# Performance work log

Measured on AMD Instinct MI355X. Metric: run time of the kernel, lower is better.

Reference implementation:

```python
import jax, jax.numpy as jnp
import numpy as np

N_NODES = 100000
N_PART = 5000
N_EDGES = 1000000
D_NODE = 128
D_PART = 128
D_ATT = 20


def setup_inputs() -> dict:
    key = jax.random.key(0)
    ks = jax.random.split(key, 20)
    inp = {
        "nodes_hidden": jax.random.normal(ks[0], (N_NODES, D_NODE), jnp.float32),
        "particles_hidden": jax.random.normal(ks[1], (N_PART, D_PART), jnp.float32),
        "global_rep": jax.random.normal(ks[2], (N_PART, D_NODE), jnp.float32),
        "src": jax.random.randint(ks[3], (N_EDGES,), 0, N_NODES, jnp.int32),
        "dst": jax.random.randint(ks[4], (N_EDGES,), 0, N_PART, jnp.int32),
        "key_W": jax.random.normal(ks[5], (D_NODE, D_ATT), jnp.float32) * 0.05,
        "key_b": jnp.zeros((D_ATT,), jnp.float32),
        "val_W": jax.random.normal(ks[6], (D_NODE, D_PART), jnp.float32) * 0.05,
        "val_b": jnp.zeros((D_PART,), jnp.float32),
        "q_W": jax.random.normal(ks[7], (D_PART + D_NODE, D_ATT), jnp.float32) * 0.05,
        "q_b": jnp.zeros((D_ATT,), jnp.float32),
        "W_ih": jax.random.normal(ks[8], (3 * D_PART, D_PART), jnp.float32) * 0.05,
        "W_hh": jax.random.normal(ks[9], (3 * D_PART, D_PART), jnp.float32) * 0.05,
        "b_ih": jnp.zeros((3 * D_PART,), jnp.float32),
        "b_hh": jnp.zeros((3 * D_PART,), jnp.float32),
        "ln_g": jnp.ones((D_PART,), jnp.float32),
        "ln_b": jnp.zeros((D_PART,), jnp.float32),
        "mlp_W1": jax.random.normal(ks[10], (D_PART, 64), jnp.float32) * 0.05,
        "mlp_b1": jnp.zeros((64,), jnp.float32),
        "mlp_W2": jax.random.normal(ks[11], (64, D_PART), jnp.float32) * 0.05,
        "mlp_b2": jnp.zeros((D_PART,), jnp.float32),
    }
    return inp


def reference(nodes_hidden, particles_hidden, global_rep, src, dst,
              key_W, key_b, val_W, val_b, q_W, q_b,
              W_ih, W_hh, b_ih, b_hh, ln_g, ln_b,
              mlp_W1, mlp_b1, mlp_W2, mlp_b2):
    norm = jnp.float32(1.0) / jnp.sqrt(jnp.float32(D_ATT))
    keys = nodes_hidden @ key_W + key_b          # [N, 20]
    vals = nodes_hidden @ val_W + val_b          # [N, P]
    q_in = jnp.concatenate([particles_hidden, global_rep], axis=1)
    query = q_in @ q_W + q_b                     # [Np, 20]

    # per-edge raw attention (ReLU'd copy in edges.data is unused downstream)
    att = jnp.sum(keys[src] * query[dst], axis=1) * norm     # [E]
    msg = att[:, None] * vals[src]                            # [E, P]
    weighted_sum = jax.ops.segment_sum(msg, dst, num_segments=particles_hidden.shape[0])

    # GRUCell(input=weighted_sum, hidden=particles_hidden), torch semantics
    gi = weighted_sum @ W_ih.T + b_ih
    gh = particles_hidden @ W_hh.T + b_hh
    i_r, i_z, i_n = jnp.split(gi, 3, axis=1)
    h_r, h_z, h_n = jnp.split(gh, 3, axis=1)
    r = jax.nn.sigmoid(i_r + h_r)
    z = jax.nn.sigmoid(i_z + h_z)
    n = jnp.tanh(i_n + r * h_n)
    h_new = (1.0 - z) * n + z * particles_hidden

    # LayerNorm (eps=1e-5)
    mu = jnp.mean(h_new, axis=-1, keepdims=True)
    var = jnp.mean(jnp.square(h_new - mu), axis=-1, keepdims=True)
    ln = (h_new - mu) * jax.lax.rsqrt(var + 1e-5) * ln_g + ln_b

    mlp_out = jax.nn.relu(ln @ mlp_W1 + mlp_b1) @ mlp_W2 + mlp_b2
    return particles_hidden + mlp_out
```

## Files before the change

kernel.cpp:

```cpp
#include <hip/hip_runtime.h>
#include <hip/hip_fp16.h>
#include <math.h>

#define N_NODES 100000
#define N_PART  5000
#define N_EDGES 1000000
#define D_NODE  128
#define D_PART  128
#define D_ATT   20
#define NBLK    128
#define EPB     ((N_EDGES + NBLK - 1) / NBLK)
#define TPV3    10

__device__ __forceinline__ float sigmoid_(float x) { return 1.f / (1.f + __expf(-x)); }
__device__ __forceinline__ float tanh_(float x)    { return 1.f - 2.f / (__expf(2.f * x) + 1.f); }

__global__ __launch_bounds__(256) void build_wbig_dot_kernel(
    const float* __restrict__ valW, const float* __restrict__ Wih,
    float* __restrict__ Wbig)
{
    __shared__ float s_a[32][128];
    __shared__ float s_b[64][128];
    int kt = blockIdx.x / 6, jt = blockIdx.x % 6;
    int k0 = kt * 32, j0 = jt * 64;
    int t = threadIdx.x;

    for (int f = t; f < 32 * 32; f += 256) {
        int r = f >> 5, c4 = (f & 31) * 4;
        *(float4*)&s_a[r][c4] = *(const float4*)(valW + (size_t)(k0 + r) * 128 + c4);
    }
    for (int f = t; f < 64 * 32; f += 256) {
        int r = f >> 5, c4 = (f & 31) * 4;
        *(float4*)&s_b[r][c4] = *(const float4*)(Wih + (size_t)(j0 + r) * 128 + c4);
    }
    __syncthreads();

    #pragma unroll
    for (int f = 0; f < 8; f++) {
        int idx = t + f * 256;
        int kk = idx >> 6, jj = idx & 63;
        float acc = 0.f;
        #pragma unroll 8
        for (int m = 0; m < 128; m++) acc += s_a[kk][m] * s_b[jj][m];
        Wbig[(size_t)(k0 + kk) * 512 + j0 + jj] = acc;
    }
    if (jt == 0) {
        for (int f = t; f < 32 * 128; f += 256) {
            int kk = f >> 7, jj = 384 + (f & 127);
            Wbig[(size_t)(k0 + kk) * 512 + jj] = 0.f;
        }
    }
}

__global__ __launch_bounds__(256) void build_wbig_copy_kernel(
    const float* __restrict__ Whh, float* __restrict__ Wbig)
{
    int idx = blockIdx.x * 256 + threadIdx.x;
    int kp = idx >> 9;
    int j = idx & 511;
    float v = 0.f;
    if (j < 256)       v = Whh[j * 128 + kp];
    else if (j >= 384) v = Whh[(j - 128) * 128 + kp];
    Wbig[(size_t)(128 + kp) * 512 + j] = v;
}

__global__ __launch_bounds__(256) void build_bvec_kernel(
    const float* __restrict__ valb, const float* __restrict__ Wih,
    float* __restrict__ bvec)
{
    int c = blockIdx.x * 256 + threadIdx.x;
    if (c < 384) {
        float acc = 0.f;
        #pragma unroll 8
        for (int m = 0; m < 128; m++) acc += valb[m] * Wih[c * 128 + m];
        bvec[c] = acc;
    }
}

__global__ __launch_bounds__(256) void nodes_to_half_kernel(
    const float* __restrict__ nodes, __half* __restrict__ nh)
{
    int i = blockIdx.x * 256 + threadIdx.x;
    if (i < N_NODES * D_NODE / 4) {
        float4 v = ((const float4*)nodes)[i];
        __half2 a = __floats2half2_rn(v.x, v.y);
        __half2 b = __floats2half2_rn(v.z, v.w);
        ((__half2*)nh)[i * 2]     = a;
        ((__half2*)nh)[i * 2 + 1] = b;
    }
}

__global__ __launch_bounds__(256) void query_qk_v2(
    const float* __restrict__ ph, const float* __restrict__ gr,
    const float* __restrict__ qW, const float* __restrict__ qb,
    const float* __restrict__ keyW, const float* __restrict__ keyb,
    float* __restrict__ qk, float* __restrict__ qoff)
{
    __shared__ float s_in[32][256];
    __shared__ float s_qW[256 * 20];
    __shared__ float s_kWT[20][128];
    __shared__ float s_q[32][20];

    int t = threadIdx.x;
    int pbase = blockIdx.x * 32;

    for (int f = t; f < 32 * 64; f += 256) {
        int pl = f >> 6, c4 = (f & 63) * 4;
        int p = min(pbase + pl, N_PART - 1);
        float4 v;
        if (c4 < 128) v = *(const float4*)(ph + (size_t)p * 128 + c4);
        else          v = *(const float4*)(gr + (size_t)p * 128 + (c4 - 128));
        *(float4*)&s_in[pl][c4] = v;
    }
    for (int f = t; f < 1280; f += 256)
        *(float4*)&s_qW[f * 4] = *(const float4*)(qW + f * 4);
    for (int f = t; f < 2560; f += 256) {
        int j = f / 20, a = f % 20;
        s_kWT[a][j] = keyW[f];
    }
    __syncthreads();

    for (int idx = t; idx < 32 * 20; idx += 256) {
        int pl = idx / 20, a = idx % 20;
        float acc = qb[a];
        #pragma unroll 8
        for (int k = 0; k < 256; k++) acc += s_in[pl][k] * s_qW[k * 20 + a];
        s_q[pl][a] = acc;
    }
    __syncthreads();

    for (int idx = t; idx < 32 * 128; idx += 256) {
        int pl = idx >> 7, j = idx & 127;
        int p = pbase + pl;
        if (p < N_PART) {
            float acc = 0.f;
            #pragma unroll
            for (int a = 0; a < D_ATT; a++) acc += s_kWT[a][j] * s_q[pl][a];
            qk[(size_t)p * 128 + j] = acc;
        }
    }
    if (t < 32) {
        int p = pbase + t;
        if (p < N_PART) {
            float o = 0.f;
            #pragma unroll
            for (int a = 0; a < D_ATT; a++) o += keyb[a] * s_q[t][a];
            qoff[p] = o;
        }
    }
}

__global__ __launch_bounds__(256) void block_hist_kernel(
    const int* __restrict__ dst, int* __restrict__ blockhist)
{
    __shared__ int h[N_PART];
    int b = blockIdx.x;
    for (int i = threadIdx.x; i < N_PART; i += 256) h[i] = 0;
    __syncthreads();
    int beg = b * EPB, end = min(beg + EPB, N_EDGES);
    for (int e = beg + threadIdx.x; e < end; e += 256)
        atomicAdd(&h[dst[e]], 1);
    __syncthreads();
    for (int i = threadIdx.x; i < N_PART; i += 256)
        blockhist[(size_t)b * N_PART + i] = h[i];
}

__global__ __launch_bounds__(256) void colscan_kernel(
    int* __restrict__ blockhist, int* __restrict__ totals)
{
    int i = blockIdx.x * 256 + threadIdx.x;
    if (i >= N_PART) return;
    int run = 0;
    for (int b = 0; b < NBLK; b++) {
        size_t idx = (size_t)b * N_PART + i;
        int v = blockhist[idx];
        blockhist[idx] = run;
        run += v;
    }
    totals[i] = run;
}

__global__ __launch_bounds__(256) void scan_kernel(
    const int* __restrict__ totals, int* __restrict__ offsets)
{
    __shared__ int ss[256];
    int t = threadIdx.x;
    const int CH = 20;
    int beg = t * CH;
    int end = min(beg + CH, N_PART);
    int lsum = 0;
    for (int i = beg; i < end; i++) lsum += totals[i];
    ss[t] = lsum;
    __syncthreads();
    for (int off = 1; off < 256; off <<= 1) {
        int v = (t >= off) ? ss[t - off] : 0;
        __syncthreads();
        ss[t] += v;
        __syncthreads();
    }
    int base = ss[t] - lsum;
    for (int i = beg; i < end; i++) {
        offsets[i] = base;
        base += totals[i];
    }
    if (t == 0) offsets[N_PART] = N_EDGES;
}

__global__ __launch_bounds__(256) void scatter_sorted_kernel(
    const int* __restrict__ src, const int* __restrict__ dst,
    const int* __restrict__ offsets, const int* __restrict__ blockhist,
    int* __restrict__ ssrc)
{
    __shared__ int cur[N_PART];
    int b = blockIdx.x;
    for (int i = threadIdx.x; i < N_PART; i += 256)
        cur[i] = offsets[i] + blockhist[(size_t)b * N_PART + i];
    __syncthreads();
    int beg = b * EPB, end = min(beg + EPB, N_EDGES);
    for (int e = beg + threadIdx.x; e < end; e += 256) {
        int d = dst[e];
        int pos = atomicAdd(&cur[d], 1);
        ssrc[pos] = src[e];
    }
}

__global__ __launch_bounds__(256) void edge_agg_f16(
    const __half* __restrict__ nh, const float* __restrict__ qk,
    const float* __restrict__ qoff,
    const int* __restrict__ offsets, const int* __restrict__ ssrc,
    float* __restrict__ agg, float* __restrict__ att_sum)
{
    const float norm = 0.22360679774997896f;
    int p = blockIdx.x;
    int tid = threadIdx.x;
    int lane = tid & 63;
    int wave = tid >> 6;
    int lane16 = lane & 15;
    int col8 = lane16 * 8;

    float4 q0 = *(const float4*)(qk + (size_t)p * 128 + col8);
    float4 q1 = *(const float4*)(qk + (size_t)p * 128 + col8 + 4);
    float qo = qoff[p];
    int beg = offsets[p];
    int n = offsets[p + 1] - beg;

    float4 a0 = {0.f, 0.f, 0.f, 0.f};
    float4 a1 = {0.f, 0.f, 0.f, 0.f};
    float asum = 0.f;

    int i = wave * 8 + (lane >> 4);
    for (; i + 4 < n; i += 32) {
        int sA = ssrc[beg + i];
        int sB = ssrc[beg + i + 4];
        float4 rawA = *(const float4*)(nh + (size_t)sA * 128 + col8);
        float4 rawB = *(const float4*)(nh + (size_t)sB * 128 + col8);
        const __half2* hA = (const __half2*)&rawA;
        const __half2* hB = (const __half2*)&rawB;
        float2 xa0 = __half22float2(hA[0]), xa1 = __half22float2(hA[1]);
        float2 xa2 = __half22float2(hA[2]), xa3 = __half22float2(hA[3]);
        float2 xb0 = __half22float2(hB[0]), xb1 = __half22float2(hB[1]);
        float2 xb2 = __half22float2(hB[2]), xb3 = __half22float2(hB[3]);
        float dA = xa0.x * q0.x + xa0.y * q0.y + xa1.x * q0.z + xa1.y * q0.w
                 + xa2.x * q1.x + xa2.y * q1.y + xa3.x * q1.z + xa3.y * q1.w;
        float dB = xb0.x * q0.x + xb0.y * q0.y + xb1.x * q0.z + xb1.y * q0.w
                 + xb2.x * q1.x + xb2.y * q1.y + xb3.x * q1.z + xb3.y * q1.w;
        #pragma unroll
        for (int off = 1; off <= 8; off <<= 1) {
            dA += __shfl_xor(dA, off, 64);
            dB += __shfl_xor(dB, off, 64);
        }
        float attA = (dA + qo) * norm;
        float attB = (dB + qo) * norm;
        a0.x += attA * xa0.x + attB * xb0.x;
        a0.y += attA * xa0.y + attB * xb0.y;
        a0.z += attA * xa1.x + attB * xb1.x;
        a0.w += attA * xa1.y + attB * xb1.y;
        a1.x += attA * xa2.x + attB * xb2.x;
        a1.y += attA * xa2.y + attB * xb2.y;
        a1.z += attA * xa3.x + attB * xb3.x;
        a1.w += attA * xa3.y + attB * xb3.y;
        asum += attA + attB;
    }
    if (i < n) {
        int sA = ssrc[beg + i];
        float4 rawA = *(const float4*)(nh + (size_t)sA * 128 + col8);
        const __half2* hA = (const __half2*)&rawA;
        float2 xa0 = __half22float2(hA[0]), xa1 = __half22float2(hA[1]);
        float2 xa2 = __half22float2(hA[2]), xa3 = __half22float2(hA[3]);
        float dA = xa0.x * q0.x + xa0.y * q0.y + xa1.x * q0.z + xa1.y * q0.w
                 + xa2.x * q1.x + xa2.y * q1.y + xa3.x * q1.z + xa3.y * q1.w;
        #pragma unroll
        for (int off = 1; off <= 8; off <<= 1) dA += __shfl_xor(dA, off, 64);
        float attA = (dA + qo) * norm;
        a0.x += attA * xa0.x; a0.y += attA * xa0.y;
        a0.z += attA * xa1.x; a0.w += attA * xa1.y;
        a1.x += attA * xa2.x; a1.y += attA * xa2.y;
        a1.z += attA * xa3.x; a1.w += attA * xa3.y;
        asum += attA;
    }

    #pragma unroll
    for (int off = 16; off <= 32; off <<= 1) {
        a0.x += __shfl_xor(a0.x, off, 64);
        a0.y += __shfl_xor(a0.y, off, 64);
        a0.z += __shfl_xor(a0.z, off, 64);
        a0.w += __shfl_xor(a0.w, off, 64);
        a1.x += __shfl_xor(a1.x, off, 64);
        a1.y += __shfl_xor(a1.y, off, 64);
        a1.z += __shfl_xor(a1.z, off, 64);
        a1.w += __shfl_xor(a1.w, off, 64);
        asum += __shfl_xor(asum, off, 64);
    }

    __shared__ float s_part[4][128];
    __shared__ float s_as[4];
    if (lane < 16) {
        *(float4*)&s_part[wave][col8]     = a0;
        *(float4*)&s_part[wave][col8 + 4] = a1;
        if (lane == 0) s_as[wave] = asum;
    }
    __syncthreads();

    if (tid < 128) {
        float v = s_part[0][tid] + s_part[1][tid] + s_part[2][tid] + s_part[3][tid];
        agg[(size_t)p * 128 + tid] = v;
        if (tid == 0) att_sum[p] = s_as[0] + s_as[1] + s_as[2] + s_as[3];
    }
}

__global__ __launch_bounds__(256) void edge_agg_f32(
    const float* __restrict__ nodes, const float* __restrict__ qk,
    const float* __restrict__ qoff,
    const int* __restrict__ offsets, const int* __restrict__ ssrc,
    float* __restrict__ agg, float* __restrict__ att_sum)
{
    const float norm = 0.22360679774997896f;
    int p = blockIdx.x;
    int tid = threadIdx.x;
    int lane = tid & 63;
    int wave = tid >> 6;
    int half = lane >> 5;
    int colq = (lane & 31) * 4;

    const float4 q = *(const float4*)(qk + (size_t)p * 128 + colq);
    float qo = qoff[p];
    int beg = offsets[p], end = offsets[p + 1];
    int n = end - beg;
    int np = (n + 1) >> 1;
    int npfull = n >> 1;

    float4 a = {0.f, 0.f, 0.f, 0.f};
    float asum = 0.f;

    int pi = wave;
    for (; pi + 12 < npfull; pi += 16) {
        int e0 = beg + 2 * pi + half;
        int s0 = ssrc[e0];
        int s1 = ssrc[e0 + 8];
        int s2 = ssrc[e0 + 16];
        int s3 = ssrc[e0 + 24];
        float4 x0 = *(const float4*)(nodes + (size_t)s0 * 128 + colq);
        float4 x1 = *(const float4*)(nodes + (size_t)s1 * 128 + colq);
        float4 x2 = *(const float4*)(nodes + (size_t)s2 * 128 + colq);
        float4 x3 = *(const float4*)(nodes + (size_t)s3 * 128 + colq);
        float d0 = x0.x * q.x + x0.y * q.y + x0.z * q.z + x0.w * q.w;
        float d1 = x1.x * q.x + x1.y * q.y + x1.z * q.z + x1.w * q.w;
        float d2 = x2.x * q.x + x2.y * q.y + x2.z * q.z + x2.w * q.w;
        float d3 = x3.x * q.x + x3.y * q.y + x3.z * q.z + x3.w * q.w;
        #pragma unroll
        for (int off = 1; off <= 16; off <<= 1) {
            d0 += __shfl_xor(d0, off, 64);
            d1 += __shfl_xor(d1, off, 64);
            d2 += __shfl_xor(d2, off, 64);
            d3 += __shfl_xor(d3, off, 64);
        }
        float t0 = (d0 + qo) * norm;
        float t1 = (d1 + qo) * norm;
        float t2 = (d2 + qo) * norm;
        float t3 = (d3 + qo) * norm;
        a.x += t0 * x0.x + t1 * x1.x + t2 * x2.x + t3 * x3.x;
        a.y += t0 * x0.y + t1 * x1.y + t2 * x2.y + t3 * x3.y;
        a.z += t0 * x0.z + t1 * x1.z + t2 * x2.z + t3 * x3.z;
        a.w += t0 * x0.w + t1 * x1.w + t2 * x2.w + t3 * x3.w;
        asum += t0 + t1 + t2 + t3;
    }
    for (; pi < np; pi += 4) {
        int e0 = beg + 2 * pi;
        bool has1 = (e0 + 1 < end);
        int s0 = ssrc[e0];
        int s1 = has1 ? ssrc[e0 + 1] : s0;
        int s = half ? s1 : s0;
        float4 x = *(const float4*)(nodes + (size_t)s * 128 + colq);
        float d = x.x * q.x + x.y * q.y + x.z * q.z + x.w * q.w;
        #pragma unroll
        for (int off = 1; off <= 16; off <<= 1) d += __shfl_xor(d, off, 64);
        float att = (d + qo) * norm;
        if (half && !has1) att = 0.f;
        a.x += att * x.x; a.y += att * x.y; a.z += att * x.z; a.w += att * x.w;
        asum += att;
    }

    a.x += __shfl_xor(a.x, 32, 64);
    a.y += __shfl_xor(a.y, 32, 64);
    a.z += __shfl_xor(a.z, 32, 64);
    a.w += __shfl_xor(a.w, 32, 64);
    asum += __shfl_xor(asum, 32, 64);

    __shared__ float s_acc[4][128];
    __shared__ float s_as[4];
    if (lane < 32) {
        *(float4*)&s_acc[wave][colq] = a;
        if (lane == 0) s_as[wave] = asum;
    }
    __syncthreads();

    if (tid < 128) {
        float v = s_acc[0][tid] + s_acc[1][tid] + s_acc[2][tid] + s_acc[3][tid];
        agg[(size_t)p * 128 + tid] = v;
        if (tid == 0) att_sum[p] = s_as[0] + s_as[1] + s_as[2] + s_as[3];
    }
}

__global__ __launch_bounds__(256) void gru_fused_v4(
    const float* __restrict__ agg, const float* __restrict__ att_sum,
    const float* __restrict__ ph,
    const float* __restrict__ Wbig, const float* __restrict__ bvec,
    const float* __restrict__ bih, const float* __restrict__ bhh,
    const float* __restrict__ lng, const float* __restrict__ lnb,
    const float* __restrict__ W1, const float* __restrict__ b1,
    const float* __restrict__ W2, const float* __restrict__ b2,
    float* __restrict__ out)
{
    __shared__ float s_in[TPV3][256];
    __shared__ float s_acc[TPV3][512];
    __shared__ float s_ln[TPV3][128];
    __shared__ float s_hid[TPV3][64];

    int t = threadIdx.x;
    int pbase = blockIdx.x * TPV3;

    for (int f = t; f < TPV3 * 64; f += 256) {
        int pl = f >> 6, c4 = (f & 63) * 4;
        int p = pbase + pl;
        float4 v;
        if (c4 < 128) v = *(const float4*)(agg + (size_t)p * 128 + c4);
        else          v = *(const float4*)(ph + (size_t)p * 128 + (c4 - 128));
        *(float4*)&s_in[pl][c4] = v;
    }

    int jq = t & 127;
    int j4 = jq * 4;
    int pg = t >> 7;
    float4 cb, bv;
    if (j4 < 256) {
        float4 bi = *(const float4*)(bih + j4);
        float4 bh = *(const float4*)(bhh + j4);
        cb.x = bi.x + bh.x; cb.y = bi.y + bh.y; cb.z = bi.z + bh.z; cb.w = bi.w + bh.w;
        bv = *(const float4*)(bvec + j4);
    } else if (j4 < 384) {
        cb = *(const float4*)(bih + j4);
        bv = *(const float4*)(bvec + j4);
    } else {
        cb = *(const float4*)(bhh + (j4 - 128));
        bv.x = bv.y = bv.z = bv.w = 0.f;
    }
    float4 acc[5];
    #pragma unroll
    for (int i = 0; i < 5; i++) {
        float as = att_sum[pbase + pg * 5 + i];
        acc[i].x = cb.x + as * bv.x;
        acc[i].y = cb.y + as * bv.y;
        acc[i].z = cb.z + as * bv.z;
        acc[i].w = cb.w + as * bv.w;
    }
    __syncthreads();

    #pragma unroll 4
    for (int k = 0; k < 256; k++) {
        float4 w = *(const float4*)(Wbig + (size_t)k * 512 + j4);
        #pragma unroll
        for (int i = 0; i < 5; i++) {
            float x = s_in[pg * 5 + i][k];
            acc[i].x += x * w.x; acc[i].y += x * w.y;
            acc[i].z += x * w.z; acc[i].w += x * w.w;
        }
    }

    #pragma unroll
    for (int i = 0; i < 5; i++)
        *(float4*)&s_acc[pg * 5 + i][j4] = acc[i];
    __syncthreads();

    for (int idx = t; idx < TPV3 * 32; idx += 256) {
        int pl = idx >> 5, q = idx & 31;
        int c4 = q * 4;
        float4 r4 = *(const float4*)&s_acc[pl][c4];
        float4 z4 = *(const float4*)&s_acc[pl][128 + c4];
        float4 i4 = *(const float4*)&s_acc[pl][256 + c4];
        float4 n4 = *(const float4*)&s_acc[pl][384 + c4];
        float4 h4 = *(const float4*)&s_in[pl][128 + c4];
        float r0 = sigmoid_(r4.x), r1 = sigmoid_(r4.y), r2 = sigmoid_(r4.z), r3 = sigmoid_(r4.w);
        float z0 = sigmoid_(z4.x), z1 = sigmoid_(z4.y), z2 = sigmoid_(z4.z), z3 = sigmoid_(z4.w);
        float n0 = tanh_(i4.x + r0 * n4.x), n1 = tanh_(i4.y + r1 * n4.y);
        float n2 = tanh_(i4.z + r2 * n4.z), n3 = tanh_(i4.w + r3 * n4.w);
        float4 hn;
        hn.x = (1.f - z0) * n0 + z0 * h4.x;
        hn.y = (1.f - z1) * n1 + z1 * h4.y;
        hn.z = (1.f - z2) * n2 + z2 * h4.z;
        hn.w = (1.f - z3) * n3 + z3 * h4.w;
        *(float4*)&s_ln[pl][c4] = hn;
    }
    __syncthreads();

    {
        int wv = t >> 6, l = t & 63;
        for (int pl = wv; pl < TPV3; pl += 4) {
            float v0 = s_ln[pl][l * 2], v1 = s_ln[pl][l * 2 + 1];
            float sum = v0 + v1, sq = v0 * v0 + v1 * v1;
            #pragma unroll
            for (int off = 1; off <= 32; off <<= 1) {
                sum += __shfl_xor(sum, off, 64);
                sq  += __shfl_xor(sq, off, 64);
            }
            float mu = sum * (1.f / 128.f);
            float var = sq * (1.f / 128.f) - mu * mu;
            float rstd = rsqrtf(var + 1e-5f);
            s_ln[pl][l * 2]     = (v0 - mu) * rstd * lng[l * 2] + lnb[l * 2];
            s_ln[pl][l * 2 + 1] = (v1 - mu) * rstd * lng[l * 2 + 1] + lnb[l * 2 + 1];
        }
    }
    __syncthreads();

    for (int idx = t; idx < TPV3 * 64; idx += 256) {
        int pl = idx >> 6, u = idx & 63;
        float a0 = b1[u];
        #pragma unroll 4
        for (int k = 0; k < 128; k++) a0 += s_ln[pl][k] * W1[k * 64 + u];
        s_hid[pl][u] = fmaxf(a0, 0.f);
    }
    __syncthreads();

    for (int idx = t; idx < TPV3 * 32; idx += 256) {
        int pl = idx >> 5, q = idx & 31;
        int c4 = q * 4;
        float4 o = *(const float4*)(b2 + c4);
        #pragma unroll 4
        for (int u = 0; u < 64; u++) {
            float av = s_hid[pl][u];
            float4 w = *(const float4*)(W2 + u * 128 + c4);
            o.x += av * w.x; o.y += av * w.y; o.z += av * w.z; o.w += av * w.w;
        }
        float4 h4 = *(const float4*)&s_in[pl][128 + c4];
        float4 res;
        res.x = h4.x + o.x; res.y = h4.y + o.y;
        res.z = h4.z + o.z; res.w = h4.w + o.w;
        *(float4*)(out + (size_t)(pbase + pl) * 128 + c4) = res;
    }
}

extern "C" void kernel_launch(void* const* d_in, const int* in_sizes, int n_in,
                              void* d_out, int out_size, void* d_ws, size_t ws_size,
                              hipStream_t stream) {
    const float* nodes = (const float*)d_in[0];
    const float* ph    = (const float*)d_in[1];
    const float* gr    = (const float*)d_in[2];
    const int*   src   = (const int*)d_in[3];
    const int*   dst   = (const int*)d_in[4];
    const float* keyW  = (const float*)d_in[5];
    const float* keyb  = (const float*)d_in[6];
    const float* valW  = (const float*)d_in[7];
    const float* valb  = (const float*)d_in[8];
    const float* qW    = (const float*)d_in[9];
    const float* qb    = (const float*)d_in[10];
    const float* Wih   = (const float*)d_in[11];
    const float* Whh   = (const float*)d_in[12];
    const float* bih   = (const float*)d_in[13];
    const float* bhh   = (const float*)d_in[14];
    const float* lng   = (const float*)d_in[15];
    const float* lnb   = (const float*)d_in[16];
    const float* W1    = (const float*)d_in[17];
    const float* b1    = (const float*)d_in[18];
    const float* W2    = (const float*)d_in[19];
    const float* b2    = (const float*)d_in[20];
    float* out = (float*)d_out;

    float* ws_f      = (float*)d_ws;
    float* qk        = ws_f;
    float* qoff      = qk + 640000;
    float* agg       = qoff + 5008;
    float* att_sum   = agg + 640000;
    float* Wbig      = att_sum + 5008;
    float* bvec      = Wbig + 131072;
    int*   totals    = (int*)(bvec + 512);
    int*   offsets   = totals + 5008;
    int*   blockhist = offsets + 5008;
    int*   ssrc      = blockhist + (size_t)NBLK * N_PART;
    __half* nodes_h  = (__half*)(ssrc + 1000000);

    size_t base_floats = 640000 + 5008 + 640000 + 5008 + 131072 + 512
                       + 5008 + 5008 + (size_t)NBLK * N_PART + 1000000;
    size_t need_f16 = base_floats * sizeof(float) + (size_t)N_NODES * D_NODE * sizeof(__half);
    bool use_f16 = (ws_size >= need_f16);

    build_wbig_dot_kernel<<<24, 256, 0, stream>>>(valW, Wih, Wbig);
    build_wbig_copy_kernel<<<256, 256, 0, stream>>>(Whh, Wbig);
    build_bvec_kernel<<<2, 256, 0, stream>>>(valb, Wih, bvec);
    query_qk_v2<<<(N_PART + 31) / 32, 256, 0, stream>>>(ph, gr, qW, qb, keyW, keyb, qk, qoff);
    block_hist_kernel<<<NBLK, 256, 0, stream>>>(dst, blockhist);
    colscan_kernel<<<(N_PART + 255) / 256, 256, 0, stream>>>(blockhist, totals);
    scan_kernel<<<1, 256, 0, stream>>>(totals, offsets);
    scatter_sorted_kernel<<<NBLK, 256, 0, stream>>>(src, dst, offsets, blockhist, ssrc);
    if (use_f16) {
        nodes_to_half_kernel<<<(N_NODES * D_NODE / 4 + 255) / 256, 256, 0, stream>>>(nodes, nodes_h);
        edge_agg_f16<<<N_PART, 256, 0, stream>>>(nodes_h, qk, qoff, offsets, ssrc, agg, att_sum);
    } else {
        edge_agg_f32<<<N_PART, 256, 0, stream>>>(nodes, qk, qoff, offsets, ssrc, agg, att_sum);
    }
    gru_fused_v4<<<N_PART / TPV3, 256, 0, stream>>>(
        agg, att_sum, ph, Wbig, bvec, bih, bhh, lng, lnb, W1, b1, W2, b2, out);
}
```

Baseline: 326.5 us.

## Merge setup kernels, fuse sort passes with grid barriers, split GRU stage

```diff
diff --git a/kernel.cpp b/kernel.cpp
--- a/kernel.cpp
+++ b/kernel.cpp
@@ -8,219 +8,222 @@
 #define D_NODE  128
 #define D_PART  128
 #define D_ATT   20
-#define NBLK    128
-#define EPB     ((N_EDGES + NBLK - 1) / NBLK)
-#define TPV3    10
+#define SORTB   128
+#define EPB     ((N_EDGES + SORTB - 1) / SORTB)
+
+#define CONV_END  12500
+#define DOT_END   (CONV_END + 192)
+#define COPY_END  (DOT_END + 256)
+#define ZF_END    (COPY_END + 64)
+#define BINIT_END (ZF_END + 2)
+#define MB_END    (BINIT_END + 128)
+#define MK_END    (MB_END + 1)
+#define SETUP_GRID MK_END
 
 __device__ __forceinline__ float sigmoid_(float x) { return 1.f / (1.f + __expf(-x)); }
 __device__ __forceinline__ float tanh_(float x)    { return 1.f - 2.f / (__expf(2.f * x) + 1.f); }
 
-__global__ __launch_bounds__(256) void build_wbig_dot_kernel(
+__global__ __launch_bounds__(256) void mega_setup(
+    const float* __restrict__ nodes, __half* __restrict__ nh, int use_f16,
     const float* __restrict__ valW, const float* __restrict__ Wih,
-    float* __restrict__ Wbig)
+    const float* __restrict__ Whh, const float* __restrict__ valb,
+    const float* __restrict__ bih, const float* __restrict__ bhh,
+    const float* __restrict__ qW, const float* __restrict__ qb,
+    const float* __restrict__ keyW, const float* __restrict__ keyb,
+    float* __restrict__ Wbig2, float* __restrict__ binit,
+    float* __restrict__ bvec4, float* __restrict__ M,
+    float* __restrict__ mkbuf)
 {
-    __shared__ float s_a[32][128];
-    __shared__ float s_b[64][128];
-    int kt = blockIdx.x / 6, jt = blockIdx.x % 6;
-    int k0 = kt * 32, j0 = jt * 64;
+    int b = blockIdx.x;
     int t = threadIdx.x;
 
-    for (int f = t; f < 32 * 32; f += 256) {
-        int r = f >> 5, c4 = (f & 31) * 4;
-        *(float4*)&s_a[r][c4] = *(const float4*)(valW + (size_t)(k0 + r) * 128 + c4);
-    }
-    for (int f = t; f < 64 * 32; f += 256) {
-        int r = f >> 5, c4 = (f & 31) * 4;
-        *(float4*)&s_b[r][c4] = *(const float4*)(Wih + (size_t)(j0 + r) * 128 + c4);
-    }
-    __syncthreads();
-
-    #pragma unroll
-    for (int f = 0; f < 8; f++) {
-        int idx = t + f * 256;
-        int kk = idx >> 6, jj = idx & 63;
+    if (b < CONV_END) {
+        if (!use_f16) return;
+        int i = b * 256 + t;
+        float4 v = ((const float4*)nodes)[i];
+        __half2 a = __floats2half2_rn(v.x, v.y);
+        __half2 c = __floats2half2_rn(v.z, v.w);
+        ((__half2*)nh)[i * 2]     = a;
+        ((__half2*)nh)[i * 2 + 1] = c;
+    } else if (b < DOT_END) {
+        int idx = (b - CONV_END) * 256 + t;
+        int k = idx / 384, c = idx % 384;
+        const float* va = valW + (size_t)k * 128;
+        const float* wb = Wih + (size_t)c * 128;
         float acc = 0.f;
         #pragma unroll 8
-        for (int m = 0; m < 128; m++) acc += s_a[kk][m] * s_b[jj][m];
-        Wbig[(size_t)(k0 + kk) * 512 + j0 + jj] = acc;
-    }
-    if (jt == 0) {
-        for (int f = t; f < 32 * 128; f += 256) {
-            int kk = f >> 7, jj = 384 + (f & 127);
-            Wbig[(size_t)(k0 + kk) * 512 + jj] = 0.f;
-        }
-    }
-}
-
-__global__ __launch_bounds__(256) void build_wbig_copy_kernel(
-    const float* __restrict__ Whh, float* __restrict__ Wbig)
-{
-    int idx = blockIdx.x * 256 + threadIdx.x;
-    int kp = idx >> 9;
-    int j = idx & 511;
-    float v = 0.f;
-    if (j < 256)       v = Whh[j * 128 + kp];
-    else if (j >= 384) v = Whh[(j - 128) * 128 + kp];
-    Wbig[(size_t)(128 + kp) * 512 + j] = v;
-}
-
-__global__ __launch_bounds__(256) void build_bvec_kernel(
-    const float* __restrict__ valb, const float* __restrict__ Wih,
-    float* __restrict__ bvec)
-{
-    int c = blockIdx.x * 256 + threadIdx.x;
-    if (c < 384) {
+        for (int m = 0; m < 128; m++) acc += va[m] * wb[m];
+        Wbig2[(size_t)k * 512 + (c & 127) * 4 + (c >> 7)] = acc;
+    } else if (b < COPY_END) {
+        int idx = (b - DOT_END) * 256 + t;
+        int kp = idx >> 9, rem = idx & 511;
+        int j = rem >> 2, g = rem & 3;
+        float v = 0.f;
+        if (g < 2)       v = Whh[(size_t)(g * 128 + j) * 128 + kp];
+        else if (g == 3) v = Whh[(size_t)(256 + j) * 128 + kp];
+        Wbig2[(size_t)(128 + kp) * 512 + rem] = v;
+    } else if (b < ZF_END) {
+        int idx = (b - COPY_END) * 256 + t;
+        int k = idx >> 7, j = idx & 127;
+        Wbig2[(size_t)k * 512 + j * 4 + 3] = 0.f;
+    } else if (b < BINIT_END) {
+        int idx = (b - ZF_END) * 256 + t;
+        int j = idx >> 2, g = idx & 3;
+        float bi;
+        if (g == 0)      bi = bih[j] + bhh[j];
+        else if (g == 1) bi = bih[128 + j] + bhh[128 + j];
+        else if (g == 2) bi = bih[256 + j];
+        else             bi = bhh[256 + j];
+        binit[idx] = bi;
+        float bv = 0.f;
+        if (g < 3) {
+            const float* wr = Wih + (size_t)(g * 128 + j) * 128;
+            #pragma unroll 8
+            for (int m = 0; m < 128; m++) bv += valb[m] * wr[m];
+        }
+        bvec4[idx] = bv;
+    } else if (b < MB_END) {
+        int idx = (b - BINIT_END) * 256 + t;
+        int k = idx >> 7, j = idx & 127;
+        const float* qr = qW + k * 20;
+        const float* kr = keyW + j * 20;
         float acc = 0.f;
-        #pragma unroll 8
-        for (int m = 0; m < 128; m++) acc += valb[m] * Wih[c * 128 + m];
-        bvec[c] = acc;
-    }
-}
-
-__global__ __launch_bounds__(256) void nodes_to_half_kernel(
-    const float* __restrict__ nodes, __half* __restrict__ nh)
-{
-    int i = blockIdx.x * 256 + threadIdx.x;
-    if (i < N_NODES * D_NODE / 4) {
-        float4 v = ((const float4*)nodes)[i];
-        __half2 a = __floats2half2_rn(v.x, v.y);
-        __half2 b = __floats2half2_rn(v.z, v.w);
-        ((__half2*)nh)[i * 2]     = a;
-        ((__half2*)nh)[i * 2 + 1] = b;
-    }
-}
-
-__global__ __launch_bounds__(256) void query_qk_v2(
-    const float* __restrict__ ph, const float* __restrict__ gr,
-    const float* __restrict__ qW, const float* __restrict__ qb,
-    const float* __restrict__ keyW, const float* __restrict__ keyb,
-    float* __restrict__ qk, float* __restrict__ qoff)
-{
-    __shared__ float s_in[32][256];
-    __shared__ float s_qW[256 * 20];
-    __shared__ float s_kWT[20][128];
-    __shared__ float s_q[32][20];
-
-    int t = threadIdx.x;
-    int pbase = blockIdx.x * 32;
-
-    for (int f = t; f < 32 * 64; f += 256) {
-        int pl = f >> 6, c4 = (f & 63) * 4;
-        int p = min(pbase + pl, N_PART - 1);
-        float4 v;
-        if (c4 < 128) v = *(const float4*)(ph + (size_t)p * 128 + c4);
-        else          v = *(const float4*)(gr + (size_t)p * 128 + (c4 - 128));
-        *(float4*)&s_in[pl][c4] = v;
-    }
-    for (int f = t; f < 1280; f += 256)
-        *(float4*)&s_qW[f * 4] = *(const float4*)(qW + f * 4);
-    for (int f = t; f < 2560; f += 256) {
-        int j = f / 20, a = f % 20;
-        s_kWT[a][j] = keyW[f];
-    }
-    __syncthreads();
-
-    for (int idx = t; idx < 32 * 20; idx += 256) {
-        int pl = idx / 20, a = idx % 20;
-        float acc = qb[a];
-        #pragma unroll 8
-        for (int k = 0; k < 256; k++) acc += s_in[pl][k] * s_qW[k * 20 + a];
-        s_q[pl][a] = acc;
-    }
-    __syncthreads();
-
-    for (int idx = t; idx < 32 * 128; idx += 256) {
-        int pl = idx >> 7, j = idx & 127;
-        int p = pbase + pl;
-        if (p < N_PART) {
+        #pragma unroll
+        for (int a = 0; a < D_ATT; a++) acc += qr[a] * kr[a];
+        M[idx] = acc;
+    } else {
+        {
+            float acc = 0.f;
+            const float* qr = qW + t * 20;
+            #pragma unroll
+            for (int a = 0; a < D_ATT; a++) acc += qr[a] * keyb[a];
+            mkbuf[t] = acc;
+        }
+        if (t < 128) {
+            float acc = 0.f;
+            const float* kr = keyW + t * 20;
+            #pragma unroll
+            for (int a = 0; a < D_ATT; a++) acc += qb[a] * kr[a];
+            mkbuf[260 + t] = acc;
+        }
+        if (t == 0) {
             float acc = 0.f;
             #pragma unroll
-            for (int a = 0; a < D_ATT; a++) acc += s_kWT[a][j] * s_q[pl][a];
-            qk[(size_t)p * 128 + j] = acc;
-        }
-    }
-    if (t < 32) {
-        int p = pbase + t;
-        if (p < N_PART) {
-            float o = 0.f;
-            #pragma unroll
-            for (int a = 0; a < D_ATT; a++) o += keyb[a] * s_q[t][a];
+            for (int a = 0; a < D_ATT; a++) acc += qb[a] * keyb[a];
+            mkbuf[256] = acc;
+        }
+    }
+}
+
+__device__ __forceinline__ void gridbar(int* bar, int nblk) {
+    __syncthreads();
+    if (threadIdx.x == 0) {
+        __threadfence();
+        atomicAdd(bar, 1);
+        while (__hip_atomic_load(bar, __ATOMIC_ACQUIRE, __HIP_MEMORY_SCOPE_AGENT) < nblk) {}
+        __threadfence();
+    }
+    __syncthreads();
+}
+
+__global__ __launch_bounds__(256) void phase2_kernel(
+    const int* __restrict__ src, const int* __restrict__ dst,
+    const float* __restrict__ ph, const float* __restrict__ gr,
+    const float* __restrict__ M, const float* __restrict__ mkbuf,
+    int* __restrict__ blockhist, int* __restrict__ totals,
+    int* __restrict__ offsets, int* __restrict__ ssrc,
+    float* __restrict__ qk, float* __restrict__ qoff,
+    int* __restrict__ bar)
+{
+    __shared__ char smem[20000];
+    int t = threadIdx.x;
+
+    if (blockIdx.x < SORTB) {
+        int b = blockIdx.x;
+        int* h = (int*)smem;
+        for (int i = t; i < N_PART; i += 256) h[i] = 0;
+        __syncthreads();
+        int beg = b * EPB, end = min(beg + EPB, N_EDGES);
+        for (int e = beg + t; e < end; e += 256)
+            atomicAdd(&h[dst[e]], 1);
+        __syncthreads();
+        for (int i = t; i < N_PART; i += 256)
+            blockhist[(size_t)b * N_PART + i] = h[i];
+        gridbar(&bar[0], SORTB);
+
+        int gid = b * 256 + t;
+        if (gid < N_PART) {
+            int run = 0;
+            for (int bb = 0; bb < SORTB; bb++) {
+                size_t idx = (size_t)bb * N_PART + gid;
+                int v = blockhist[idx];
+                blockhist[idx] = run;
+                run += v;
+            }
+            totals[gid] = run;
+        }
+        gridbar(&bar[1], SORTB);
+
+        if (b == 0) {
+            __shared__ int ss[256];
+            const int CH = 20;
+            int sbeg = t * CH;
+            int send = min(sbeg + CH, N_PART);
+            int lsum = 0;
+            for (int i = sbeg; i < send; i++) lsum += totals[i];
+            ss[t] = lsum;
+            __syncthreads();
+            for (int off = 1; off < 256; off <<= 1) {
+                int v = (t >= off) ? ss[t - off] : 0;
+                __syncthreads();
+                ss[t] += v;
+                __syncthreads();
+            }
+            int base = ss[t] - lsum;
+            for (int i = sbeg; i < send; i++) {
+                offsets[i] = base;
+                base += totals[i];
+            }
+            if (t == 0) offsets[N_PART] = N_EDGES;
+        }
+        gridbar(&bar[2], SORTB);
+
+        for (int i = t; i < N_PART; i += 256)
+            h[i] = offsets[i] + blockhist[(size_t)b * N_PART + i];
+        __syncthreads();
+        for (int e = beg + t; e < end; e += 256) {
+            int d = dst[e];
+            int pos = atomicAdd(&h[d], 1);
+            ssrc[pos] = src[e];
+        }
+    } else {
+        float (*s_in)[256] = (float(*)[256])smem;
+        int pbase = (blockIdx.x - SORTB) * 8;
+        for (int f = t; f < 8 * 64; f += 256) {
+            int pl = f >> 6, c4 = (f & 63) * 4;
+            int p = pbase + pl;
+            float4 v;
+            if (c4 < 128) v = *(const float4*)(ph + (size_t)p * 128 + c4);
+            else          v = *(const float4*)(gr + (size_t)p * 128 + (c4 - 128));
+            *(float4*)&s_in[pl][c4] = v;
+        }
+        __syncthreads();
+        int pl = t >> 5, jq = t & 31;
+        int j4 = jq * 4;
+        int p = pbase + pl;
+        float4 acc = *(const float4*)(mkbuf + 260 + j4);
+        #pragma unroll 4
+        for (int k = 0; k < 256; k++) {
+            float x = s_in[pl][k];
+            float4 w = *(const float4*)(M + (size_t)k * 128 + j4);
+            acc.x += x * w.x; acc.y += x * w.y; acc.z += x * w.z; acc.w += x * w.w;
+        }
+        *(float4*)(qk + (size_t)p * 128 + j4) = acc;
+        if (jq == 0) {
+            float o = mkbuf[256];
+            for (int k = 0; k < 256; k++) o += s_in[pl][k] * mkbuf[k];
             qoff[p] = o;
         }
-    }
-}
-
-__global__ __launch_bounds__(256) void block_hist_kernel(
-    const int* __restrict__ dst, int* __restrict__ blockhist)
-{
-    __shared__ int h[N_PART];
-    int b = blockIdx.x;
-    for (int i = threadIdx.x; i < N_PART; i += 256) h[i] = 0;
-    __syncthreads();
-    int beg = b * EPB, end = min(beg + EPB, N_EDGES);
-    for (int e = beg + threadIdx.x; e < end; e += 256)
-        atomicAdd(&h[dst[e]], 1);
-    __syncthreads();
-    for (int i = threadIdx.x; i < N_PART; i += 256)
-        blockhist[(size_t)b * N_PART + i] = h[i];
-}
-
-__global__ __launch_bounds__(256) void colscan_kernel(
-    int* __restrict__ blockhist, int* __restrict__ totals)
-{
-    int i = blockIdx.x * 256 + threadIdx.x;
-    if (i >= N_PART) return;
-    int run = 0;
-    for (int b = 0; b < NBLK; b++) {
-        size_t idx = (size_t)b * N_PART + i;
-        int v = blockhist[idx];
-        blockhist[idx] = run;
-        run += v;
-    }
-    totals[i] = run;
-}
-
-__global__ __launch_bounds__(256) void scan_kernel(
-    const int* __restrict__ totals, int* __restrict__ offsets)
-{
-    __shared__ int ss[256];
-    int t = threadIdx.x;
-    const int CH = 20;
-    int beg = t * CH;
-    int end = min(beg + CH, N_PART);
-    int lsum = 0;
-    for (int i = beg; i < end; i++) lsum += totals[i];
-    ss[t] = lsum;
-    __syncthreads();
-    for (int off = 1; off < 256; off <<= 1) {
-        int v = (t >= off) ? ss[t - off] : 0;
-        __syncthreads();
-        ss[t] += v;
-        __syncthreads();
-    }
-    int base = ss[t] - lsum;
-    for (int i = beg; i < end; i++) {
-        offsets[i] = base;
-        base += totals[i];
-    }
-    if (t == 0) offsets[N_PART] = N_EDGES;
-}
-
-__global__ __launch_bounds__(256) void scatter_sorted_kernel(
-    const int* __restrict__ src, const int* __restrict__ dst,
-    const int* __restrict__ offsets, const int* __restrict__ blockhist,
-    int* __restrict__ ssrc)
-{
-    __shared__ int cur[N_PART];
-    int b = blockIdx.x;
-    for (int i = threadIdx.x; i < N_PART; i += 256)
-        cur[i] = offsets[i] + blockhist[(size_t)b * N_PART + i];
-    __syncthreads();
-    int beg = b * EPB, end = min(beg + EPB, N_EDGES);
-    for (int e = beg + threadIdx.x; e < end; e += 256) {
-        int d = dst[e];
-        int pos = atomicAdd(&cur[d], 1);
-        ssrc[pos] = src[e];
     }
 }
 
@@ -421,25 +424,18 @@
     }
 }
 
-__global__ __launch_bounds__(256) void gru_fused_v4(
+__global__ __launch_bounds__(256) void gru_gemm(
     const float* __restrict__ agg, const float* __restrict__ att_sum,
     const float* __restrict__ ph,
-    const float* __restrict__ Wbig, const float* __restrict__ bvec,
-    const float* __restrict__ bih, const float* __restrict__ bhh,
-    const float* __restrict__ lng, const float* __restrict__ lnb,
-    const float* __restrict__ W1, const float* __restrict__ b1,
-    const float* __restrict__ W2, const float* __restrict__ b2,
-    float* __restrict__ out)
+    const float* __restrict__ Wbig2, const float* __restrict__ binit,
+    const float* __restrict__ bvec4, float* __restrict__ hnew)
 {
-    __shared__ float s_in[TPV3][256];
-    __shared__ float s_acc[TPV3][512];
-    __shared__ float s_ln[TPV3][128];
-    __shared__ float s_hid[TPV3][64];
-
+    __shared__ float s_in[8][256];
     int t = threadIdx.x;
-    int pbase = blockIdx.x * TPV3;
-
-    for (int f = t; f < TPV3 * 64; f += 256) {
+    int pg = blockIdx.x >> 2, cg = blockIdx.x & 3;
+    int pbase = pg * 8;
+
+    for (int f = t; f < 8 * 64; f += 256) {
         int pl = f >> 6, c4 = (f & 63) * 4;
         int p = pbase + pl;
         float4 v;
@@ -448,114 +444,93 @@
         *(float4*)&s_in[pl][c4] = v;
     }
 
-    int jq = t & 127;
-    int j4 = jq * 4;
-    int pg = t >> 7;
-    float4 cb, bv;
-    if (j4 < 256) {
-        float4 bi = *(const float4*)(bih + j4);
-        float4 bh = *(const float4*)(bhh + j4);
-        cb.x = bi.x + bh.x; cb.y = bi.y + bh.y; cb.z = bi.z + bh.z; cb.w = bi.w + bh.w;
-        bv = *(const float4*)(bvec + j4);
-    } else if (j4 < 384) {
-        cb = *(const float4*)(bih + j4);
-        bv = *(const float4*)(bvec + j4);
-    } else {
-        cb = *(const float4*)(bhh + (j4 - 128));
-        bv.x = bv.y = bv.z = bv.w = 0.f;
-    }
-    float4 acc[5];
-    #pragma unroll
-    for (int i = 0; i < 5; i++) {
-        float as = att_sum[pbase + pg * 5 + i];
-        acc[i].x = cb.x + as * bv.x;
-        acc[i].y = cb.y + as * bv.y;
-        acc[i].z = cb.z + as * bv.z;
-        acc[i].w = cb.w + as * bv.w;
-    }
+    int pl = t >> 5, jq = t & 31;
+    int j = cg * 32 + jq;
+    float4 bi = *(const float4*)(binit + j * 4);
+    float4 bv = *(const float4*)(bvec4 + j * 4);
+    float asum = att_sum[pbase + pl];
+    float4 acc;
+    acc.x = bi.x + asum * bv.x;
+    acc.y = bi.y + asum * bv.y;
+    acc.z = bi.z + asum * bv.z;
+    acc.w = bi.w + asum * bv.w;
     __syncthreads();
 
+    const float* wp = Wbig2 + j * 4;
     #pragma unroll 4
     for (int k = 0; k < 256; k++) {
-        float4 w = *(const float4*)(Wbig + (size_t)k * 512 + j4);
-        #pragma unroll
-        for (int i = 0; i < 5; i++) {
-            float x = s_in[pg * 5 + i][k];
-            acc[i].x += x * w.x; acc[i].y += x * w.y;
-            acc[i].z += x * w.z; acc[i].w += x * w.w;
-        }
-    }
-
+        float4 w = *(const float4*)(wp + k * 512);
+        float x = s_in[pl][k];
+        acc.x += x * w.x; acc.y += x * w.y;
+        acc.z += x * w.z; acc.w += x * w.w;
+    }
+
+    float r = sigmoid_(acc.x);
+    float z = sigmoid_(acc.y);
+    float n = tanh_(acc.z + r * acc.w);
+    float h = s_in[pl][128 + j];
+    hnew[(size_t)(pbase + pl) * 128 + j] = (1.f - z) * n + z * h;
+}
+
+__global__ __launch_bounds__(256) void epilogue_kernel(
+    const float* __restrict__ hnew, const float* __restrict__ ph,
+    const float* __restrict__ lng, const float* __restrict__ lnb,
+    const float* __restrict__ W1, const float* __restrict__ b1,
+    const float* __restrict__ W2, const float* __restrict__ b2,
+    float* __restrict__ out)
+{
+    __shared__ float s_ln[8][128];
+    __shared__ float s_hid[8][64];
+    int t = threadIdx.x;
+    int pbase = blockIdx.x * 8;
+    int pl = t >> 5, jq = t & 31;
+    int j4 = jq * 4;
+    int p = pbase + pl;
+
+    float4 hn = *(const float4*)(hnew + (size_t)p * 128 + j4);
+    float sum = hn.x + hn.y + hn.z + hn.w;
+    float sq  = hn.x * hn.x + hn.y * hn.y + hn.z * hn.z + hn.w * hn.w;
     #pragma unroll
-    for (int i = 0; i < 5; i++)
-        *(float4*)&s_acc[pg * 5 + i][j4] = acc[i];
+    for (int off = 1; off <= 16; off <<= 1) {
+        sum += __shfl_xor(sum, off, 64);
+        sq  += __shfl_xor(sq, off, 64);
+    }
+    float mu = sum * (1.f / 128.f);
+    float var = sq * (1.f / 128.f) - mu * mu;
+    float rstd = rsqrtf(var + 1e-5f);
+    {
+        float4 g4 = *(const float4*)(lng + j4);
+        float4 b4 = *(const float4*)(lnb + j4);
+        float4 ln4;
+        ln4.x = (hn.x - mu) * rstd * g4.x + b4.x;
+        ln4.y = (hn.y - mu) * rstd * g4.y + b4.y;
+        ln4.z = (hn.z - mu) * rstd * g4.z + b4.z;
+        ln4.w = (hn.w - mu) * rstd * g4.w + b4.w;
+        *(float4*)&s_ln[pl][j4] = ln4;
+    }
     __syncthreads();
 
-    for (int idx = t; idx < TPV3 * 32; idx += 256) {
-        int pl = idx >> 5, q = idx & 31;
-        int c4 = q * 4;
-        float4 r4 = *(const float4*)&s_acc[pl][c4];
-        float4 z4 = *(const float4*)&s_acc[pl][128 + c4];
-        float4 i4 = *(const float4*)&s_acc[pl][256 + c4];
-        float4 n4 = *(const float4*)&s_acc[pl][384 + c4];
-        float4 h4 = *(const float4*)&s_in[pl][128 + c4];
-        float r0 = sigmoid_(r4.x), r1 = sigmoid_(r4.y), r2 = sigmoid_(r4.z), r3 = sigmoid_(r4.w);
-        float z0 = sigmoid_(z4.x), z1 = sigmoid_(z4.y), z2 = sigmoid_(z4.z), z3 = sigmoid_(z4.w);
-        float n0 = tanh_(i4.x + r0 * n4.x), n1 = tanh_(i4.y + r1 * n4.y);
-        float n2 = tanh_(i4.z + r2 * n4.z), n3 = tanh_(i4.w + r3 * n4.w);
-        float4 hn;
-        hn.x = (1.f - z0) * n0 + z0 * h4.x;
-        hn.y = (1.f - z1) * n1 + z1 * h4.y;
-        hn.z = (1.f - z2) * n2 + z2 * h4.z;
-        hn.w = (1.f - z3) * n3 + z3 * h4.w;
-        *(float4*)&s_ln[pl][c4] = hn;
-    }
-    __syncthreads();
-
-    {
-        int wv = t >> 6, l = t & 63;
-        for (int pl = wv; pl < TPV3; pl += 4) {
-            float v0 = s_ln[pl][l * 2], v1 = s_ln[pl][l * 2 + 1];
-            float sum = v0 + v1, sq = v0 * v0 + v1 * v1;
-            #pragma unroll
-            for (int off = 1; off <= 32; off <<= 1) {
-                sum += __shfl_xor(sum, off, 64);
-                sq  += __shfl_xor(sq, off, 64);
-            }
-            float mu = sum * (1.f / 128.f);
-            float var = sq * (1.f / 128.f) - mu * mu;
-            float rstd = rsqrtf(var + 1e-5f);
-            s_ln[pl][l * 2]     = (v0 - mu) * rstd * lng[l * 2] + lnb[l * 2];
-            s_ln[pl][l * 2 + 1] = (v1 - mu) * rstd * lng[l * 2 + 1] + lnb[l * 2 + 1];
-        }
-    }
-    __syncthreads();
-
-    for (int idx = t; idx < TPV3 * 64; idx += 256) {
-        int pl = idx >> 6, u = idx & 63;
+    for (int idx = t; idx < 8 * 64; idx += 256) {
+        int pl2 = idx >> 6, u = idx & 63;
         float a0 = b1[u];
         #pragma unroll 4
-        for (int k = 0; k < 128; k++) a0 += s_ln[pl][k] * W1[k * 64 + u];
-        s_hid[pl][u] = fmaxf(a0, 0.f);
+        for (int k = 0; k < 128; k++) a0 += s_ln[pl2][k] * W1[k * 64 + u];
+        s_hid[pl2][u] = fmaxf(a0, 0.f);
     }
     __syncthreads();
 
-    for (int idx = t; idx < TPV3 * 32; idx += 256) {
-        int pl = idx >> 5, q = idx & 31;
-        int c4 = q * 4;
-        float4 o = *(const float4*)(b2 + c4);
-        #pragma unroll 4
-        for (int u = 0; u < 64; u++) {
-            float av = s_hid[pl][u];
-            float4 w = *(const float4*)(W2 + u * 128 + c4);
-            o.x += av * w.x; o.y += av * w.y; o.z += av * w.z; o.w += av * w.w;
-        }
-        float4 h4 = *(const float4*)&s_in[pl][128 + c4];
-        float4 res;
-        res.x = h4.x + o.x; res.y = h4.y + o.y;
-        res.z = h4.z + o.z; res.w = h4.w + o.w;
-        *(float4*)(out + (size_t)(pbase + pl) * 128 + c4) = res;
-    }
+    float4 o = *(const float4*)(b2 + j4);
+    #pragma unroll 4
+    for (int u = 0; u < 64; u++) {
+        float av = s_hid[pl][u];
+        float4 w = *(const float4*)(W2 + u * 128 + j4);
+        o.x += av * w.x; o.y += av * w.y; o.z += av * w.z; o.w += av * w.w;
+    }
+    float4 h4 = *(const float4*)(ph + (size_t)p * 128 + j4);
+    float4 res;
+    res.x = h4.x + o.x; res.y = h4.y + o.y;
+    res.z = h4.z + o.z; res.w = h4.w + o.w;
+    *(float4*)(out + (size_t)p * 128 + j4) = res;
 }
 
 extern "C" void kernel_launch(void* const* d_in, const int* in_sizes, int n_in,
@@ -584,38 +559,44 @@
     const float* b2    = (const float*)d_in[20];
     float* out = (float*)d_out;
 
-    float* ws_f      = (float*)d_ws;
-    float* qk        = ws_f;
-    float* qoff      = qk + 640000;
-    float* agg       = qoff + 5008;
-    float* att_sum   = agg + 640000;
-    float* Wbig      = att_sum + 5008;
-    float* bvec      = Wbig + 131072;
-    int*   totals    = (int*)(bvec + 512);
-    int*   offsets   = totals + 5008;
-    int*   blockhist = offsets + 5008;
-    int*   ssrc      = blockhist + (size_t)NBLK * N_PART;
-    __half* nodes_h  = (__half*)(ssrc + 1000000);
-
-    size_t base_floats = 640000 + 5008 + 640000 + 5008 + 131072 + 512
-                       + 5008 + 5008 + (size_t)NBLK * N_PART + 1000000;
-    size_t need_f16 = base_floats * sizeof(float) + (size_t)N_NODES * D_NODE * sizeof(__half);
-    bool use_f16 = (ws_size >= need_f16);
-
-    build_wbig_dot_kernel<<<24, 256, 0, stream>>>(valW, Wih, Wbig);
-    build_wbig_copy_kernel<<<256, 256, 0, stream>>>(Whh, Wbig);
-    build_bvec_kernel<<<2, 256, 0, stream>>>(valb, Wih, bvec);
-    query_qk_v2<<<(N_PART + 31) / 32, 256, 0, stream>>>(ph, gr, qW, qb, keyW, keyb, qk, qoff);
-    block_hist_kernel<<<NBLK, 256, 0, stream>>>(dst, blockhist);
-    colscan_kernel<<<(N_PART + 255) / 256, 256, 0, stream>>>(blockhist, totals);
-    scan_kernel<<<1, 256, 0, stream>>>(totals, offsets);
-    scatter_sorted_kernel<<<NBLK, 256, 0, stream>>>(src, dst, offsets, blockhist, ssrc);
+    float* ws_f    = (float*)d_ws;
+    float* qk      = ws_f;
+    float* qoff    = qk + 640000;
+    float* agg     = qoff + 5008;
+    float* att_sum = agg + 640000;
+    float* Wbig2   = att_sum + 5008;
+    float* binit   = Wbig2 + 131072;
+    float* bvec4   = binit + 512;
+    float* mkbuf   = bvec4 + 512;
+    float* M_      = mkbuf + 400;
+    int*   totals  = (int*)(M_ + 32768);
+    int*   offsets = totals + 5008;
+    int*   bar     = offsets + 5008;
+    int*   blockhist = bar + 16;
+    int*   ssrc    = blockhist + (size_t)SORTB * N_PART;
+    __half* nodes_h = (__half*)(ssrc + 1000000);
+
+    size_t base_floats = 640000 + 5008 + 640000 + 5008 + 131072 + 512 + 512 + 400
+                       + 32768 + 5008 + 5008 + 16 + (size_t)SORTB * N_PART + 1000000;
+    size_t need_f16 = base_floats * 4 + (size_t)N_NODES * D_NODE * sizeof(__half);
+    int use_f16 = (ws_size >= need_f16) ? 1 : 0;
+
+    hipMemsetAsync(bar, 0, 16 * sizeof(int), stream);
+
+    mega_setup<<<SETUP_GRID, 256, 0, stream>>>(
+        nodes, nodes_h, use_f16, valW, Wih, Whh, valb, bih, bhh,
+        qW, qb, keyW, keyb, Wbig2, binit, bvec4, M_, mkbuf);
+
+    phase2_kernel<<<SORTB + 625, 256, 0, stream>>>(
+        src, dst, ph, gr, M_, mkbuf, blockhist, totals, offsets, ssrc, qk, qoff, bar);
+
     if (use_f16) {
-        nodes_to_half_kernel<<<(N_NODES * D_NODE / 4 + 255) / 256, 256, 0, stream>>>(nodes, nodes_h);
         edge_agg_f16<<<N_PART, 256, 0, stream>>>(nodes_h, qk, qoff, offsets, ssrc, agg, att_sum);
     } else {
         edge_agg_f32<<<N_PART, 256, 0, stream>>>(nodes, qk, qoff, offsets, ssrc, agg, att_sum);
     }
-    gru_fused_v4<<<N_PART / TPV3, 256, 0, stream>>>(
-        agg, att_sum, ph, Wbig, bvec, bih, bhh, lng, lnb, W1, b1, W2, b2, out);
-}
+
+    gru_gemm<<<2500, 256, 0, stream>>>(agg, att_sum, ph, Wbig2, binit, bvec4, qk);
+
+    epilogue_kernel<<<625, 256, 0, stream>>>(qk, ph, lng, lnb, W1, b1, W2, b2, out);
+}
```

After: 437.5 us. 34.0% more time.
